# Performance work log

Measured on AMD Instinct MI355X. Metric: run time of the kernel, lower is better.

Reference implementation:

```python
import jax, jax.numpy as jnp
import numpy as np

N, H, W, C = 4, 64, 64, 256
G, K = 8, 3
GC = C // G
P = K * K
PAD = 1
BN_EPS = 1e-3  # ultralytics Conv uses BatchNorm2d(eps=0.001)


def setup_inputs() -> dict:
    key = jax.random.key(0)
    ks = jax.random.split(key, 8)
    return {
        "x": jax.random.normal(ks[0], (N, H, W, C), jnp.float32),
        # depthwise conv weight (OIHW with I=1, feature_group_count=C)
        "dw_w": jax.random.normal(ks[1], (C, 1, K, K), jnp.float32) * 0.1,
        "bn_gamma": jnp.ones((C,), jnp.float32),
        "bn_beta": jnp.zeros((C,), jnp.float32),
        "bn_mean": jnp.zeros((C,), jnp.float32),
        "bn_var": jnp.ones((C,), jnp.float32),
        # offset/mask heads are zero-init in torch; use small random weights so
        # sampling locations are nontrivial but stay near the kernel grid
        "W_off": jax.random.normal(ks[2], (C, G * P * 2), jnp.float32) * 0.01,
        "b_off": jnp.zeros((G * P * 2,), jnp.float32),
        "W_mask": jax.random.normal(ks[3], (C, G * P), jnp.float32) * 0.01,
        "b_mask": jnp.zeros((G * P,), jnp.float32),
        "W_in": jax.random.normal(ks[4], (C, C), jnp.float32) / np.sqrt(C).astype(np.float32),
        "b_in": jnp.zeros((C,), jnp.float32),
        "W_out": jax.random.normal(ks[5], (C, C), jnp.float32) / np.sqrt(C).astype(np.float32),
        "b_out": jnp.zeros((C,), jnp.float32),
    }


def _grid_sample(img, grid):
    # img: (B, gc, Hi, Wi); grid: (B, L, P, 2) in [-1,1], (x,y) order.
    # Matches torch grid_sample(mode='bilinear', padding_mode='zeros', align_corners=False).
    B, gc, Hi, Wi = img.shape
    x = (grid[..., 0] + 1.0) * (Wi * 0.5) - 0.5
    y = (grid[..., 1] + 1.0) * (Hi * 0.5) - 0.5
    x0 = jnp.floor(x).astype(jnp.int32)
    y0 = jnp.floor(y).astype(jnp.int32)
    tx = x - x0
    ty = y - y0
    flat = img.reshape(B, gc, Hi * Wi)
    L, Pp = grid.shape[1], grid.shape[2]

    def tap(xi, yi, w):
        valid = (xi >= 0) & (xi < Wi) & (yi >= 0) & (yi < Hi)
        idx = jnp.clip(yi, 0, Hi - 1) * Wi + jnp.clip(xi, 0, Wi - 1)
        v = jnp.take_along_axis(flat, idx.reshape(B, 1, L * Pp), axis=2)
        v = v.reshape(B, gc, L, Pp)
        return v * (w * valid)[:, None]

    return (tap(x0, y0, (1 - tx) * (1 - ty))
            + tap(x0 + 1, y0, tx * (1 - ty))
            + tap(x0, y0 + 1, (1 - tx) * ty)
            + tap(x0 + 1, y0 + 1, tx * ty))


def _dcnv3_core(xp, offset, mask):
    # xp: (N,H,W,C) projected input; offset: (N,H,W,G*P*2); mask: (N,H,W,G*P)
    xpad = jnp.pad(xp, ((0, 0), (PAD, PAD), (PAD, PAD), (0, 0)))
    Hi, Wi = H + 2 * PAD, W + 2 * PAD
    # reference points on the padded grid, normalized to [0,1]
    start = (K - 1) // 2 + 0.5  # dilation=1, stride=1
    ref_y = (start + jnp.arange(H, dtype=jnp.float32)) / Hi
    ref_x = (start + jnp.arange(W, dtype=jnp.float32)) / Wi
    ref = jnp.stack(jnp.broadcast_arrays(ref_x[None, :], ref_y[:, None]), -1)  # (H,W,2) (x,y)
    # kernel dilation grid; torch meshgrid('ij') over (kw,kh) -> point p = iw*K + ih
    xv = jnp.arange(K, dtype=jnp.float32) - ((K - 1) // 2)
    gx, gy = jnp.meshgrid(xv / Wi, xv / Hi, indexing='ij')
    kgrid = jnp.stack([gx, gy], -1).reshape(P, 2)  # identical per group
    off = offset.reshape(N, H, W, G, P, 2) / jnp.array([Wi, Hi], jnp.float32)
    loc = ref[None, :, :, None, None, :] + kgrid[None, None, None, None] + off  # (N,H,W,G,P,2)
    sg = 2.0 * loc - 1.0
    # regroup channels-last input to (N*G, GC, Hi, Wi); channel c = g*GC + d
    img = xpad.reshape(N, Hi * Wi, G, GC).transpose(0, 2, 3, 1).reshape(N * G, GC, Hi, Wi)
    sgrid = sg.reshape(N, H * W, G, P, 2).transpose(0, 2, 1, 3, 4).reshape(N * G, H * W, P, 2)
    samp = _grid_sample(img, sgrid)  # (N*G, GC, L, P)
    m = mask.reshape(N, H * W, G, P).transpose(0, 2, 1, 3).reshape(N * G, 1, H * W, P)
    out = (samp * m).sum(-1)  # (N*G, GC, L)
    return out.reshape(N, C, H * W).transpose(0, 2, 1).reshape(N, H, W, C)


def reference(x, dw_w, bn_gamma, bn_beta, bn_mean, bn_var, W_off, b_off,
              W_mask, b_mask, W_in, b_in, W_out, b_out):
    x_proj = x @ W_in + b_in
    # depthwise 3x3 conv + BN (eval) + SiLU (ultralytics Conv)
    xc = x.transpose(0, 3, 1, 2)
    y = jax.lax.conv_general_dilated(
        xc, dw_w, (1, 1), ((PAD, PAD), (PAD, PAD)),
        feature_group_count=C, dimension_numbers=('NCHW', 'OIHW', 'NCHW'))
    scale = bn_gamma / jnp.sqrt(bn_var + BN_EPS)
    y = (y - bn_mean[None, :, None, None]) * scale[None, :, None, None] + bn_beta[None, :, None, None]
    y = y * jax.nn.sigmoid(y)
    x1 = y.transpose(0, 2, 3, 1)  # (N,H,W,C)
    offset = x1 @ W_off + b_off
    mlog = (x1 @ W_mask + b_mask).reshape(N, H, W, G, P)
    mask = jax.nn.softmax(mlog, axis=-1).reshape(N, H, W, G * P)
    out = _dcnv3_core(x_proj, offset, mask)
    return out @ W_out + b_out
```

## Files before the change

### kernel.cpp

```cpp
#include <hip/hip_runtime.h>
#include <math.h>

#define NPIX 16384
#define CC 256
#define OFFW 144
#define MSKW 72

typedef unsigned short ushortT;
typedef __attribute__((ext_vector_type(4))) float f32x4;
typedef __attribute__((ext_vector_type(8))) __bf16 bf16x8;
typedef __attribute__((ext_vector_type(8))) unsigned short u16x8;
typedef __attribute__((ext_vector_type(4))) unsigned int u32x4;

__device__ __forceinline__ float bf2f(ushortT u) {
    union { unsigned u; float f; } x; x.u = ((unsigned)u) << 16; return x.f;
}
__device__ __forceinline__ ushortT f2bf(float f) {
    union { float f; unsigned u; } x; x.f = f;
    unsigned u = x.u;
    return (ushortT)((u + 0x7FFFu + ((u >> 16) & 1u)) >> 16);
}
__device__ __forceinline__ float bflo(unsigned u) { return __uint_as_float(u << 16); }
__device__ __forceinline__ float bfhi(unsigned u) { return __uint_as_float(u & 0xFFFF0000u); }

typedef __attribute__((address_space(3))) char lds_char;
typedef __attribute__((address_space(1))) char glb_char;
__device__ __forceinline__ void gload_lds16(const void* g, void* l) {
    __builtin_amdgcn_global_load_lds((const glb_char*)g, (lds_char*)l, 16, 0, 0);
}

__global__ __launch_bounds__(256) void k_wt(
    const float* __restrict__ W_in, const float* __restrict__ W_out,
    const float* __restrict__ W_off, const float* __restrict__ W_mask,
    const float* __restrict__ b_in, const float* __restrict__ b_out,
    const float* __restrict__ b_off, const float* __restrict__ b_mask,
    ushortT* __restrict__ Wt, float* __restrict__ biasb)
{
    const int idx = blockIdx.x * 256 + threadIdx.x;
    const int slot = idx >> 16;
    const int rem = idx & 65535;
    const int n = rem >> 8, k = rem & 255;
    float v;
    if (slot == 0)      v = W_in[k * 256 + n];
    else if (slot == 1) v = W_out[k * 256 + n];
    else {
        if (n < OFFW)             v = W_off[k * OFFW + n];
        else if (n < OFFW + MSKW) v = W_mask[k * MSKW + (n - OFFW)];
        else                      v = 0.f;
    }
    Wt[idx] = f2bf(v);
    if (n == 0) {
        float b;
        if (slot == 0)      b = b_in[k];
        else if (slot == 1) b = b_out[k];
        else                b = (k < OFFW) ? b_off[k] : (k < OFFW + MSKW ? b_mask[k - OFFW] : 0.f);
        biasb[slot * 256 + k] = b;
    }
}

__global__ __launch_bounds__(512, 4) void k_fused_in(
    const float* __restrict__ x, const float* __restrict__ dw_w,
    const float* __restrict__ bn_gamma, const float* __restrict__ bn_beta,
    const float* __restrict__ bn_mean, const float* __restrict__ bn_var,
    const ushortT* __restrict__ Wt, const float* __restrict__ biasb,
    ushortT* __restrict__ xpb, ushortT* __restrict__ omb)
{
    __shared__ __align__(16) ushortT xA[32 * 256];
    __shared__ __align__(16) ushortT x1s[32 * 256];
    const int tid = threadIdx.x;
    const int b0 = blockIdx.x;
    const int lb = (b0 & 7) * 64 + (b0 >> 3);
    const int base = lb * 32;
    const int n = base >> 12, h = (base >> 6) & 63, bw0 = base & 63;

    {
        const int c = tid & 255, half = tid >> 8;
        float wreg[9];
        #pragma unroll
        for (int k = 0; k < 9; ++k) wreg[k] = dw_w[c * 9 + k];
        const float scale = bn_gamma[c] * rsqrtf(bn_var[c] + 1e-3f);
        const float mean = bn_mean[c], beta = bn_beta[c];
        const bool hv0 = h >= 1, hv2 = h <= 62;
        const float* r0 = x + ((size_t)(n * 64 + h - 1) * 64) * 256 + c;
        const float* r1 = x + ((size_t)(n * 64 + h) * 64) * 256 + c;
        const float* r2 = x + ((size_t)(n * 64 + h + 1) * 64) * 256 + c;
        const int w0 = bw0 + half * 16;
        float a0, a1, a2, e0, e1, e2;
        if (w0 - 1 >= 0) {
            a0 = hv0 ? r0[(w0 - 1) * 256] : 0.f;
            a1 = r1[(w0 - 1) * 256];
            a2 = hv2 ? r2[(w0 - 1) * 256] : 0.f;
        } else { a0 = a1 = a2 = 0.f; }
        e0 = hv0 ? r0[w0 * 256] : 0.f;
        e1 = r1[w0 * 256];
        e2 = hv2 ? r2[w0 * 256] : 0.f;
        #pragma unroll
        for (int i = 0; i < 16; ++i) {
            const int w = w0 + i;
            float d0, d1, d2;
            if (w + 1 < 64) {
                d0 = hv0 ? r0[(w + 1) * 256] : 0.f;
                d1 = r1[(w + 1) * 256];
                d2 = hv2 ? r2[(w + 1) * 256] : 0.f;
            } else { d0 = d1 = d2 = 0.f; }
            const float accv = a0 * wreg[0] + e0 * wreg[1] + d0 * wreg[2]
                             + a1 * wreg[3] + e1 * wreg[4] + d1 * wreg[5]
                             + a2 * wreg[6] + e2 * wreg[7] + d2 * wreg[8];
            const float yv = (accv - mean) * scale + beta;
            const float s = yv / (1.f + __expf(-yv));
            const int row = half * 16 + i;
            const int sb = (row * 512 + c * 2) ^ ((row & 7) << 4);
            *(ushortT*)((char*)x1s + sb) = f2bf(s);
            *(ushortT*)((char*)xA + sb) = f2bf(e1);
            a0 = e0; a1 = e1; a2 = e2;
            e0 = d0; e1 = d1; e2 = d2;
        }
    }
    __syncthreads();

    const int lane = tid & 63, wave = tid >> 6;
    const int gemm = wave >> 2, wc = wave & 3;
    const ushortT* As = gemm ? x1s : xA;
    const ushortT* Bt = Wt + (gemm ? 2 * 65536 : 0);
    const float* bias = biasb + (gemm ? 512 : 0);
    ushortT* Cout = gemm ? omb : xpb;

    f32x4 acc[2][4];
    #pragma unroll
    for (int m = 0; m < 2; ++m)
        #pragma unroll
        for (int nn = 0; nn < 4; ++nn) acc[m][nn] = (f32x4){0.f, 0.f, 0.f, 0.f};

    #pragma unroll
    for (int k0 = 0; k0 < 256; k0 += 32) {
        bf16x8 af[2], bb[4];
        #pragma unroll
        for (int m = 0; m < 2; ++m) {
            const int row = m * 16 + (lane & 15);
            af[m] = *(const bf16x8*)((const char*)As + row * 512 +
                     (((k0 + (lane >> 4) * 8) * 2) ^ ((row & 7) << 4)));
        }
        #pragma unroll
        for (int nn = 0; nn < 4; ++nn) {
            const int ncol = wc * 64 + nn * 16 + (lane & 15);
            bb[nn] = *(const bf16x8*)(Bt + (size_t)ncol * 256 + k0 + (lane >> 4) * 8);
        }
        #pragma unroll
        for (int m = 0; m < 2; ++m)
            #pragma unroll
            for (int nn = 0; nn < 4; ++nn)
                acc[m][nn] = __builtin_amdgcn_mfma_f32_16x16x32_bf16(af[m], bb[nn], acc[m][nn], 0, 0, 0);
    }

    const int rbase = (lane >> 4) * 4, col16 = lane & 15;
    #pragma unroll
    for (int m = 0; m < 2; ++m) {
        #pragma unroll
        for (int nn = 0; nn < 4; ++nn) {
            const int col = wc * 64 + nn * 16 + col16;
            const float bj = bias[col];
            #pragma unroll
            for (int r = 0; r < 4; ++r) {
                const int row = m * 16 + rbase + r;
                Cout[(size_t)(base + row) * 256 + col] = f2bf(acc[m][nn][r] + bj);
            }
        }
    }
}

__global__ __launch_bounds__(256) void k_core(
    const ushortT* __restrict__ omb, const ushortT* __restrict__ xpb,
    ushortT* __restrict__ coreb)
{
    __shared__ __align__(16) float wtab[8][72][8];
    const int tid = threadIdx.x;
    const int b0 = blockIdx.x;
    const int lb = (b0 & 7) * 256 + (b0 >> 3);
    const int base = lb * 8;
    const int n = base >> 12, h = (base >> 6) & 63, w0 = base & 63;

    if (tid < 64) {
        const int px = tid >> 3, g = tid & 7;
        const ushortT* omp = omb + (size_t)(base + px) * 256;
        float lg[9], mx = -1e30f;
        #pragma unroll
        for (int p = 0; p < 9; ++p) { lg[p] = bf2f(omp[OFFW + g * 9 + p]); mx = fmaxf(mx, lg[p]); }
        float e[9], sum = 0.f;
        #pragma unroll
        for (int p = 0; p < 9; ++p) { e[p] = __expf(lg[p] - mx); sum += e[p]; }
        const float inv = 1.f / sum;
        #pragma unroll
        for (int p = 0; p < 9; ++p) {
            const float m = e[p] * inv;
            const unsigned opair = *(const unsigned*)(omp + (g * 9 + p) * 2);
            const float ox = bflo(opair), oy = bfhi(opair);
            const float pxc = (float)(w0 + px + p / 3) + ox;
            const float pyc = (float)(h + p % 3) + oy;
            const float xf = floorf(pxc), yf = floorf(pyc);
            const float tx = pxc - xf, ty = pyc - yf;
            const int x0 = (int)xf - 1, y0 = (int)yf - 1;
            const int x1 = x0 + 1, y1 = y0 + 1;
            const float wx0 = ((unsigned)x0 < 64u) ? (1.f - tx) : 0.f;
            const float wx1 = ((unsigned)x1 < 64u) ? tx : 0.f;
            const float wy0 = ((unsigned)y0 < 64u) ? (1.f - ty) : 0.f;
            const float wy1 = ((unsigned)y1 < 64u) ? ty : 0.f;
            const int cx0 = min(max(x0, 0), 63), cx1 = min(max(x1, 0), 63);
            const int cy0 = min(max(y0, 0), 63), cy1 = min(max(y1, 0), 63);
            float* dst = wtab[px][g * 9 + p];
            float4 idx4, wt4;
            idx4.x = __int_as_float((cy0 * 64 + cx0) * 256);
            idx4.y = __int_as_float((cy0 * 64 + cx1) * 256);
            idx4.z = __int_as_float((cy1 * 64 + cx0) * 256);
            idx4.w = __int_as_float((cy1 * 64 + cx1) * 256);
            wt4.x = m * wx0 * wy0; wt4.y = m * wx1 * wy0;
            wt4.z = m * wx0 * wy1; wt4.w = m * wx1 * wy1;
            *(float4*)dst = idx4;
            *(float4*)(dst + 4) = wt4;
        }
    }
    __syncthreads();

    const int px = tid >> 5, g = (tid >> 2) & 7, o = tid & 3;
    const ushortT* xn = xpb + (size_t)n * (4096 * 256) + g * 32 + o * 8;
    float acc[8];
    #pragma unroll
    for (int j = 0; j < 8; ++j) acc[j] = 0.f;
    #pragma unroll
    for (int p = 0; p < 9; ++p) {
        const float* wt = wtab[px][g * 9 + p];
        const int4 o4 = *(const int4*)(wt);
        const float4 w4 = *(const float4*)(wt + 4);
        const u32x4 A = *(const u32x4*)(xn + o4.x);
        const u32x4 B = *(const u32x4*)(xn + o4.y);
        const u32x4 C = *(const u32x4*)(xn + o4.z);
        const u32x4 D = *(const u32x4*)(xn + o4.w);
        #pragma unroll
        for (int i = 0; i < 4; ++i) {
            acc[2 * i]     += w4.x * bflo(A[i]) + w4.y * bflo(B[i])
                            + w4.z * bflo(C[i]) + w4.w * bflo(D[i]);
            acc[2 * i + 1] += w4.x * bfhi(A[i]) + w4.y * bfhi(B[i])
                            + w4.z * bfhi(C[i]) + w4.w * bfhi(D[i]);
        }
    }
    u16x8 cv;
    #pragma unroll
    for (int j = 0; j < 8; ++j) cv[j] = f2bf(acc[j]);
    *(u16x8*)(coreb + (size_t)(base + px) * 256 + g * 32 + o * 8) = cv;
}

__global__ __launch_bounds__(512) void k_gemm_out(
    const ushortT* __restrict__ A, const ushortT* __restrict__ Bt,
    const float* __restrict__ bias, float* __restrict__ out)
{
    __shared__ __align__(16) ushortT As[32 * 256];
    const int tid = threadIdx.x;
    const int m0 = blockIdx.x * 32;
    const int lane = tid & 63, wave = tid >> 6;

    #pragma unroll
    for (int it = 0; it < 2; ++it) {
        const int i = it * 512 + tid;
        const int row = i >> 5, ch = i & 31;
        const int sch = ch ^ (row & 7);
        gload_lds16(A + (size_t)(m0 + row) * 256 + sch * 8, (char*)As + i * 16);
    }
    asm volatile("s_waitcnt vmcnt(0)");
    __syncthreads();

    f32x4 acc[2][2];
    #pragma unroll
    for (int m = 0; m < 2; ++m)
        #pragma unroll
        for (int nn = 0; nn < 2; ++nn) acc[m][nn] = (f32x4){0.f, 0.f, 0.f, 0.f};

    #pragma unroll
    for (int k0 = 0; k0 < 256; k0 += 32) {
        bf16x8 af[2], bb[2];
        #pragma unroll
        for (int m = 0; m < 2; ++m) {
            const int row = m * 16 + (lane & 15);
            af[m] = *(const bf16x8*)((const char*)As + row * 512 +
                     (((k0 + (lane >> 4) * 8) * 2) ^ ((row & 7) << 4)));
        }
        #pragma unroll
        for (int nn = 0; nn < 2; ++nn) {
            const int ncol = wave * 32 + nn * 16 + (lane & 15);
            bb[nn] = *(const bf16x8*)(Bt + (size_t)ncol * 256 + k0 + (lane >> 4) * 8);
        }
        #pragma unroll
        for (int m = 0; m < 2; ++m)
            #pragma unroll
            for (int nn = 0; nn < 2; ++nn)
                acc[m][nn] = __builtin_amdgcn_mfma_f32_16x16x32_bf16(af[m], bb[nn], acc[m][nn], 0, 0, 0);
    }

    const int rbase = (lane >> 4) * 4, col16 = lane & 15;
    #pragma unroll
    for (int m = 0; m < 2; ++m) {
        #pragma unroll
        for (int nn = 0; nn < 2; ++nn) {
            const int col = wave * 32 + nn * 16 + col16;
            const float bj = bias[col];
            #pragma unroll
            for (int r = 0; r < 4; ++r) {
                const int row = m0 + m * 16 + rbase + r;
                out[(size_t)row * 256 + col] = acc[m][nn][r] + bj;
            }
        }
    }
}

extern "C" void kernel_launch(void* const* d_in, const int* in_sizes, int n_in,
                              void* d_out, int out_size, void* d_ws, size_t ws_size,
                              hipStream_t stream) {
    const float* x        = (const float*)d_in[0];
    const float* dw_w     = (const float*)d_in[1];
    const float* bn_gamma = (const float*)d_in[2];
    const float* bn_beta  = (const float*)d_in[3];
    const float* bn_mean  = (const float*)d_in[4];
    const float* bn_var   = (const float*)d_in[5];
    const float* W_off    = (const float*)d_in[6];
    const float* b_off    = (const float*)d_in[7];
    const float* W_mask   = (const float*)d_in[8];
    const float* b_mask   = (const float*)d_in[9];
    const float* W_in     = (const float*)d_in[10];
    const float* b_in     = (const float*)d_in[11];
    const float* W_out    = (const float*)d_in[12];
    const float* b_out    = (const float*)d_in[13];
    float* out = (float*)d_out;

    char* w = (char*)d_ws;
    ushortT* Wt    = (ushortT*)w;
    float* biasb   = (float*)(w + 393216);
    ushortT* xpb   = (ushortT*)(w + 396288);
    ushortT* omb   = (ushortT*)(w + 396288 + 8388608);
    ushortT* coreb = (ushortT*)(w + 396288 + 2 * 8388608);

    hipLaunchKernelGGL(k_wt, dim3(768), dim3(256), 0, stream,
                       W_in, W_out, W_off, W_mask, b_in, b_out, b_off, b_mask, Wt, biasb);
    hipLaunchKernelGGL(k_fused_in, dim3(512), dim3(512), 0, stream,
                       x, dw_w, bn_gamma, bn_beta, bn_mean, bn_var, Wt, biasb, xpb, omb);
    hipLaunchKernelGGL(k_core, dim3(2048), dim3(256), 0, stream,
                       omb, xpb, coreb);
    hipLaunchKernelGGL(k_gemm_out, dim3(NPIX / 32), dim3(512), 0, stream,
                       coreb, Wt + 65536, biasb + 256, out);
}
```

Baseline: 67.98 us.

## Regroup offset/mask weight columns per group and prefetch B fragments in GEMMs

The fused offset/mask weight matrix is reordered so that each group's 18 offsets and 9 mask logits sit in one contiguous 32-column block. This lets the core kernel read each group's data with four 16-byte vector loads instead of many scalar loads. Both GEMM kernels also software-pipeline the global B-fragment loads by one k-step, issuing the first load before the barrier so load latency overlaps the LDS reads and MFMAs. This costs more registers, which may reduce occupancy.

```diff
diff --git a/kernel.cpp b/kernel.cpp
--- a/kernel.cpp
+++ b/kernel.cpp
@@ -44,16 +44,20 @@
     if (slot == 0)      v = W_in[k * 256 + n];
     else if (slot == 1) v = W_out[k * 256 + n];
     else {
-        if (n < OFFW)             v = W_off[k * OFFW + n];
-        else if (n < OFFW + MSKW) v = W_mask[k * MSKW + (n - OFFW)];
-        else                      v = 0.f;
+        const int g = n >> 5, r = n & 31;
+        if (r < 18)      v = W_off[k * OFFW + g * 18 + r];
+        else if (r < 27) v = W_mask[k * MSKW + g * 9 + (r - 18)];
+        else             v = 0.f;
     }
     Wt[idx] = f2bf(v);
     if (n == 0) {
         float b;
         if (slot == 0)      b = b_in[k];
         else if (slot == 1) b = b_out[k];
-        else                b = (k < OFFW) ? b_off[k] : (k < OFFW + MSKW ? b_mask[k - OFFW] : 0.f);
+        else {
+            const int g = k >> 5, r = k & 31;
+            b = (r < 18) ? b_off[g * 18 + r] : (r < 27 ? b_mask[g * 9 + (r - 18)] : 0.f);
+        }
         biasb[slot * 256 + k] = b;
     }
 }
@@ -72,6 +76,10 @@
     const int lb = (b0 & 7) * 64 + (b0 >> 3);
     const int base = lb * 32;
     const int n = base >> 12, h = (base >> 6) & 63, bw0 = base & 63;
+
+    const int lane = tid & 63, wave = tid >> 6;
+    const int gemm = wave >> 2, wc = wave & 3;
+    const ushortT* Bt = Wt + (gemm ? 2 * 65536 : 0);
 
     {
         const int c = tid & 255, half = tid >> 8;
@@ -116,12 +124,16 @@
             e0 = d0; e1 = d1; e2 = d2;
         }
     }
+
+    bf16x8 bbp[4];
+    #pragma unroll
+    for (int nn = 0; nn < 4; ++nn) {
+        const int ncol = wc * 64 + nn * 16 + (lane & 15);
+        bbp[nn] = *(const bf16x8*)(Bt + (size_t)ncol * 256 + (lane >> 4) * 8);
+    }
     __syncthreads();
 
-    const int lane = tid & 63, wave = tid >> 6;
-    const int gemm = wave >> 2, wc = wave & 3;
     const ushortT* As = gemm ? x1s : xA;
-    const ushortT* Bt = Wt + (gemm ? 2 * 65536 : 0);
     const float* bias = biasb + (gemm ? 512 : 0);
     ushortT* Cout = gemm ? omb : xpb;
 
@@ -134,16 +146,20 @@
     #pragma unroll
     for (int k0 = 0; k0 < 256; k0 += 32) {
         bf16x8 af[2], bb[4];
+        #pragma unroll
+        for (int nn = 0; nn < 4; ++nn) bb[nn] = bbp[nn];
+        if (k0 + 32 < 256) {
+            #pragma unroll
+            for (int nn = 0; nn < 4; ++nn) {
+                const int ncol = wc * 64 + nn * 16 + (lane & 15);
+                bbp[nn] = *(const bf16x8*)(Bt + (size_t)ncol * 256 + (k0 + 32) + (lane >> 4) * 8);
+            }
+        }
         #pragma unroll
         for (int m = 0; m < 2; ++m) {
             const int row = m * 16 + (lane & 15);
             af[m] = *(const bf16x8*)((const char*)As + row * 512 +
                      (((k0 + (lane >> 4) * 8) * 2) ^ ((row & 7) << 4)));
-        }
-        #pragma unroll
-        for (int nn = 0; nn < 4; ++nn) {
-            const int ncol = wc * 64 + nn * 16 + (lane & 15);
-            bb[nn] = *(const bf16x8*)(Bt + (size_t)ncol * 256 + k0 + (lane >> 4) * 8);
         }
         #pragma unroll
         for (int m = 0; m < 2; ++m)
@@ -181,10 +197,24 @@
 
     if (tid < 64) {
         const int px = tid >> 3, g = tid & 7;
-        const ushortT* omp = omb + (size_t)(base + px) * 256;
-        float lg[9], mx = -1e30f;
-        #pragma unroll
-        for (int p = 0; p < 9; ++p) { lg[p] = bf2f(omp[OFFW + g * 9 + p]); mx = fmaxf(mx, lg[p]); }
+        const ushortT* omp = omb + (size_t)(base + px) * 256 + g * 32;
+        const u32x4 L0 = *(const u32x4*)(omp);
+        const u32x4 L1 = *(const u32x4*)(omp + 8);
+        const u32x4 L2 = *(const u32x4*)(omp + 16);
+        const u32x4 L3 = *(const u32x4*)(omp + 24);
+        unsigned opair[9];
+        #pragma unroll
+        for (int p = 0; p < 4; ++p) { opair[p] = L0[p]; opair[4 + p] = L1[p]; }
+        opair[8] = L2[0];
+        float lg[9];
+        lg[0] = bflo(L2[1]); lg[1] = bfhi(L2[1]);
+        lg[2] = bflo(L2[2]); lg[3] = bfhi(L2[2]);
+        lg[4] = bflo(L2[3]); lg[5] = bfhi(L2[3]);
+        lg[6] = bflo(L3[0]); lg[7] = bfhi(L3[0]);
+        lg[8] = bflo(L3[1]);
+        float mx = -1e30f;
+        #pragma unroll
+        for (int p = 0; p < 9; ++p) mx = fmaxf(mx, lg[p]);
         float e[9], sum = 0.f;
         #pragma unroll
         for (int p = 0; p < 9; ++p) { e[p] = __expf(lg[p] - mx); sum += e[p]; }
@@ -192,8 +222,7 @@
         #pragma unroll
         for (int p = 0; p < 9; ++p) {
             const float m = e[p] * inv;
-            const unsigned opair = *(const unsigned*)(omp + (g * 9 + p) * 2);
-            const float ox = bflo(opair), oy = bfhi(opair);
+            const float ox = bflo(opair[p]), oy = bfhi(opair[p]);
             const float pxc = (float)(w0 + px + p / 3) + ox;
             const float pyc = (float)(h + p % 3) + oy;
             const float xf = floorf(pxc), yf = floorf(pyc);
@@ -264,6 +293,12 @@
         const int sch = ch ^ (row & 7);
         gload_lds16(A + (size_t)(m0 + row) * 256 + sch * 8, (char*)As + i * 16);
     }
+    bf16x8 bbp[2];
+    #pragma unroll
+    for (int nn = 0; nn < 2; ++nn) {
+        const int ncol = wave * 32 + nn * 16 + (lane & 15);
+        bbp[nn] = *(const bf16x8*)(Bt + (size_t)ncol * 256 + (lane >> 4) * 8);
+    }
     asm volatile("s_waitcnt vmcnt(0)");
     __syncthreads();
 
@@ -276,16 +311,20 @@
     #pragma unroll
     for (int k0 = 0; k0 < 256; k0 += 32) {
         bf16x8 af[2], bb[2];
+        #pragma unroll
+        for (int nn = 0; nn < 2; ++nn) bb[nn] = bbp[nn];
+        if (k0 + 32 < 256) {
+            #pragma unroll
+            for (int nn = 0; nn < 2; ++nn) {
+                const int ncol = wave * 32 + nn * 16 + (lane & 15);
+                bbp[nn] = *(const bf16x8*)(Bt + (size_t)ncol * 256 + (k0 + 32) + (lane >> 4) * 8);
+            }
+        }
         #pragma unroll
         for (int m = 0; m < 2; ++m) {
             const int row = m * 16 + (lane & 15);
             af[m] = *(const bf16x8*)((const char*)As + row * 512 +
                      (((k0 + (lane >> 4) * 8) * 2) ^ ((row & 7) << 4)));
-        }
-        #pragma unroll
-        for (int nn = 0; nn < 2; ++nn) {
-            const int ncol = wave * 32 + nn * 16 + (lane & 15);
-            bb[nn] = *(const bf16x8*)(Bt + (size_t)ncol * 256 + k0 + (lane >> 4) * 8);
         }
         #pragma unroll
         for (int m = 0; m < 2; ++m)
```

Measured after the change: 66.96 us. No clear change (-1.5%).
